# Performance work log

Measured on AMD Instinct MI355X. Metric: run time of the kernel, lower is better.

The kernel has to match this reference:

```python
import jax, jax.numpy as jnp
import numpy as np

NEG = 0.01  # leaky_relu negative slope used throughout AttentiveFP


def _seg_softmax(logits, seg, num):
    # softmax over entries grouped by segment id (PyG softmax w/ 1e-16 eps)
    m = jax.ops.segment_max(logits, seg, num_segments=num)
    m = jnp.where(jnp.isfinite(m), m, 0.0)
    e = jnp.exp(logits - m[seg])
    s = jax.ops.segment_sum(e, seg, num_segments=num)
    return e / (s[seg] + 1e-16)


def _gru(x, h, wi, wh, bi, bh):
    # torch.nn.GRUCell math
    gi = x @ wi.T + bi
    gh = h @ wh.T + bh
    ir, iz, inn = jnp.split(gi, 3, axis=-1)
    hr, hz, hn = jnp.split(gh, 3, axis=-1)
    r = jax.nn.sigmoid(ir + hr)
    z = jax.nn.sigmoid(iz + hz)
    n = jnp.tanh(inn + r * hn)
    return (1.0 - z) * n + z * h


def _forward(x, edge_attr, mol_feats, lin1_w, lin1_b, gate_lin1_w, gate_lin2_w, gate_att_l, gate_att_r, gate_bias, grus_wi, grus_wh, grus_bi, grus_bh, atom_w, atom_att_src, atom_att_dst, atom_bias, mol_w, mol_att_src, mol_att_dst, mol_bias, lin2_w, lin2_b, fcm0_w, fcm0_b, fcm1_w, fcm1_b, fcm2_w, fcm2_b, fc0_w, fc0_b, fc1_w, fc1_b, fc2_w, fc2_b, fc3_w, fc3_b, fc4_w, fc4_b, edge_index, batch):
    N = x.shape[0]
    G = mol_feats.shape[0]
    src, dst = edge_index[0], edge_index[1]
    lrelu = lambda v: jax.nn.leaky_relu(v, NEG)
    # AttentiveFP (eval mode: dropout off)
    xh = lrelu(x @ lin1_w.T + lin1_b)  # [N,H]
    # --- GATEConv: edge-conditioned attention, add aggregation ---
    m = lrelu(jnp.concatenate([xh[src], edge_attr], axis=-1) @ gate_lin1_w.T)  # [E,H]
    a = lrelu(m @ gate_att_l + (xh @ gate_att_r)[dst])
    a = _seg_softmax(a, dst, N)
    h = jax.ops.segment_sum((m @ gate_lin2_w.T) * a[:, None], dst, num_segments=N) + gate_bias
    xh = jax.nn.relu(_gru(jax.nn.elu(h), xh, grus_wi[0], grus_wh[0], grus_bi[0], grus_bh[0]))
    # --- GATConv layers (num_layers-1 = 2, heads=1, no self loops) ---
    for l in range(2):
        xl = xh @ atom_w[l].T
        a = lrelu((xl @ atom_att_src[l])[src] + (xl @ atom_att_dst[l])[dst])
        a = _seg_softmax(a, dst, N)
        h = jax.ops.segment_sum(xl[src] * a[:, None], dst, num_segments=N) + atom_bias[l]
        xh = jax.nn.relu(_gru(jax.nn.elu(h), xh, grus_wi[1 + l], grus_wh[1 + l], grus_bi[1 + l], grus_bh[1 + l]))
    # --- attentive graph readout (num_timesteps = 3) ---
    out = jax.nn.relu(jax.ops.segment_sum(xh, batch, num_segments=G))  # [G,H]
    xm = xh @ mol_w.T            # atom-side lin (x fixed across timesteps)
    a_src = xm @ mol_att_src
    for _ in range(3):
        a = lrelu(a_src + ((out @ mol_w.T) @ mol_att_dst)[batch])
        a = _seg_softmax(a, batch, G)
        h = jax.ops.segment_sum(xm * a[:, None], batch, num_segments=G) + mol_bias
        out = jax.nn.relu(_gru(jax.nn.elu(h), out, grus_wi[3], grus_wh[3], grus_bi[3], grus_bh[3]))
    hg = out @ lin2_w.T + lin2_b  # [G,256]
    # --- mol-feature MLP branch (SiLU) ---
    hm = jax.nn.silu(mol_feats @ fcm0_w.T + fcm0_b)
    hm = jax.nn.silu(hm @ fcm1_w.T + fcm1_b)
    hm = jax.nn.silu(hm @ fcm2_w.T + fcm2_b)
    # --- fusion MLP ---
    hg = jnp.concatenate([hg, hm], axis=1)  # [G,512]
    hg = jax.nn.silu(hg @ fc0_w.T + fc0_b)
    hg = jax.nn.silu(hg @ fc1_w.T + fc1_b)
    hg = jax.nn.silu(hg @ fc2_w.T + fc2_b)
    hg = jax.nn.silu(hg @ fc3_w.T + fc3_b)
    return hg @ fc4_w.T + fc4_b  # [G,1]


def setup_inputs() -> dict:
    key = jax.random.key(0)
    ks = iter(jax.random.split(key, 64))
    def W(*shape):
        return jax.random.normal(next(ks), shape, jnp.float32) / np.float32(np.sqrt(shape[-1]))
    def B(*shape):
        return 0.02 * jax.random.normal(next(ks), shape, jnp.float32)
    N, E, G = 131072, 262144, 8192
    Fn, Fe, Fm, H = 64, 16, 200, 256
    return dict(
        x=jax.random.normal(next(ks), (N, Fn), jnp.float32),
        edge_attr=jax.random.normal(next(ks), (E, Fe), jnp.float32),
        mol_feats=jax.random.normal(next(ks), (G, Fm), jnp.float32),
        lin1_w=W(H, Fn), lin1_b=B(H),
        gate_lin1_w=W(H, H + Fe), gate_lin2_w=W(H, H),
        gate_att_l=W(H), gate_att_r=W(H), gate_bias=B(H),
        grus_wi=W(4, 3 * H, H), grus_wh=W(4, 3 * H, H), grus_bi=B(4, 3 * H), grus_bh=B(4, 3 * H),
        atom_w=W(2, H, H), atom_att_src=W(2, H), atom_att_dst=W(2, H), atom_bias=B(2, H),
        mol_w=W(H, H), mol_att_src=W(H), mol_att_dst=W(H), mol_bias=B(H),
        lin2_w=W(H, H), lin2_b=B(H),
        fcm0_w=W(H, Fm), fcm0_b=B(H), fcm1_w=W(H, H), fcm1_b=B(H), fcm2_w=W(H, H), fcm2_b=B(H),
        fc0_w=W(512, 512), fc0_b=B(512), fc1_w=W(512, 512), fc1_b=B(512),
        fc2_w=W(512, 512), fc2_b=B(512), fc3_w=W(128, 512), fc3_b=B(128),
        fc4_w=W(1, 128), fc4_b=B(1),
        edge_index=jax.random.randint(next(ks), (2, E), 0, N),
        batch=jnp.sort(jax.random.randint(next(ks), (N,), 0, G)),
    )


def reference(x, edge_attr, mol_feats, lin1_w, lin1_b, gate_lin1_w, gate_lin2_w, gate_att_l, gate_att_r, gate_bias, grus_wi, grus_wh, grus_bi, grus_bh, atom_w, atom_att_src, atom_att_dst, atom_bias, mol_w, mol_att_src, mol_att_dst, mol_bias, lin2_w, lin2_b, fcm0_w, fcm0_b, fcm1_w, fcm1_b, fcm2_w, fcm2_b, fc0_w, fc0_b, fc1_w, fc1_b, fc2_w, fc2_b, fc3_w, fc3_b, fc4_w, fc4_b, edge_index, batch):
    return _forward(x, edge_attr, mol_feats, lin1_w, lin1_b, gate_lin1_w, gate_lin2_w, gate_att_l, gate_att_r, gate_bias, grus_wi, grus_wh, grus_bi, grus_bh, atom_w, atom_att_src, atom_att_dst, atom_bias, mol_w, mol_att_src, mol_att_dst, mol_bias, lin2_w, lin2_b, fcm0_w, fcm0_b, fcm1_w, fcm1_b, fcm2_w, fcm2_b, fc0_w, fc0_b, fc1_w, fc1_b, fc2_w, fc2_b, fc3_w, fc3_b, fc4_w, fc4_b, edge_index, batch)
```

## Files before the change

kernel.cpp:

```cpp
#include <hip/hip_runtime.h>
#include <hip/hip_bf16.h>
#include <math.h>


typedef unsigned short u16;
typedef u16 u16x8 __attribute__((ext_vector_type(8)));
typedef short s16x8 __attribute__((ext_vector_type(8)));
typedef float f32x4 __attribute__((ext_vector_type(4)));

__device__ __forceinline__ float u2f(u16 u) { return __uint_as_float(((unsigned)u) << 16); }
__device__ __forceinline__ u16 f2u(float f) {
    return __builtin_bit_cast(u16, __float2bfloat16(f));
}

#define NEGS 0.01f

typedef const __attribute__((address_space(1))) unsigned gas1_t;
typedef __attribute__((address_space(3))) unsigned las3_t;
__device__ __forceinline__ void gload16(const void* g, void* l) {
    __builtin_amdgcn_global_load_lds((gas1_t*)g, (las3_t*)l, 16, 0, 0);
}

__device__ __forceinline__ unsigned fkey(float f) {
    unsigned u = __float_as_uint(f);
    return (u & 0x80000000u) ? ~u : (u | 0x80000000u);
}
__device__ __forceinline__ float funkey(unsigned k) {
    return (k & 0x80000000u) ? __uint_as_float(k ^ 0x80000000u) : __uint_as_float(~k);
}
#define KEY_NEG_INF 0x007FFFFFu

static inline int cdiv(int a, int b) { return (a + b - 1) / b; }

__global__ void fill_f32(float* p, float v, size_t n) {
    size_t i = (size_t)blockIdx.x * 256 + threadIdx.x;
    if (i < n) p[i] = v;
}
__global__ void fill_u32(unsigned* p, unsigned v, int n) {
    int i = blockIdx.x * 256 + threadIdx.x;
    if (i < n) p[i] = v;
}
__global__ void fill_km(unsigned* key, float* sum, int n) {
    int i = blockIdx.x * 256 + threadIdx.x;
    if (i < n) { key[i] = KEY_NEG_INF; sum[i] = 0.f; }
}
__global__ void copy_f2b(const float* s, u16* d, size_t n) {
    size_t i = (size_t)blockIdx.x * 256 + threadIdx.x;
    if (i < n) d[i] = f2u(s[i]);
}
__global__ void matvecT2_k(const float* W1, const float* a1, float* o1,
                           const float* W2, const float* a2, float* o2,
                           int K, int Jout) {
    int j = blockIdx.x * 256 + threadIdx.x;
    if (j < Jout) {
        float s = 0.f;
        for (int k = 0; k < K; k++) s += W1[(size_t)k * Jout + j] * a1[k];
        o1[j] = s;
    } else if (j < 2 * Jout) {
        int jj = j - Jout;
        float s = 0.f;
        for (int k = 0; k < K; k++) s += W2[(size_t)k * Jout + jj] * a2[k];
        o2[jj] = s;
    }
}
__global__ void edge_add_lrelu_max(const float* dp4, float* elog, const float* r,
                                   const int* dsti, unsigned* key, int E) {
    int i = blockIdx.x * 256 + threadIdx.x;
    if (i < E) {
        int d = dsti[i];
        float p = (dp4[i] + dp4[(size_t)E + i]) +
                  (dp4[(size_t)2 * E + i] + dp4[(size_t)3 * E + i]);
        float v = p + r[d];
        v = v > 0.f ? v : NEGS * v;
        elog[i] = v;
        atomicMax(&key[d], fkey(v));
    }
}
__global__ void pair_logit_max(float* elog, const float* s, const float* dd,
                               const int* srci, const int* dsti, unsigned* key, int E) {
    int i = blockIdx.x * 256 + threadIdx.x;
    if (i < E) {
        int d = dsti[i];
        float v = s[srci[i]] + dd[d];
        v = v > 0.f ? v : NEGS * v;
        elog[i] = v;
        atomicMax(&key[d], fkey(v));
    }
}
__global__ void node_logit_max(float* nlog, const float* asrc, const float* wg,
                               const int* batch, unsigned* key, int N) {
    int i = blockIdx.x * 256 + threadIdx.x;
    if (i < N) {
        int b = batch[i];
        float v = asrc[i] + wg[b];
        v = v > 0.f ? v : NEGS * v;
        nlog[i] = v;
        atomicMax(&key[b], fkey(v));
    }
}
__global__ void seg_exp_k(const float* logit, const int* idx, const unsigned* key,
                          float* ex, float* sum, int n) {
    int i = blockIdx.x * 256 + threadIdx.x;
    if (i < n) {
        float e = expf(logit[i] - funkey(key[idx[i]]));
        ex[i] = e;
        atomicAdd(&sum[idx[i]], e);
    }
}
__global__ void rowdot2_b(const u16* X, const float* v1, const float* v2,
                          float* o1, float* o2, int M) {
    int r = blockIdx.x * 4 + (threadIdx.x >> 6);
    int lane = threadIdx.x & 63;
    if (r >= M) return;
    ushort4 rv = *(const ushort4*)(X + (size_t)r * 256 + lane * 4);
    u16 q4[4] = {rv.x, rv.y, rv.z, rv.w};
    float p1 = 0.f, p2 = 0.f;
#pragma unroll
    for (int q = 0; q < 4; q++) {
        float xv = u2f(q4[q]);
        p1 += xv * v1[lane * 4 + q];
        if (v2) p2 += xv * v2[lane * 4 + q];
    }
    for (int off = 32; off; off >>= 1) {
        p1 += __shfl_down(p1, off);
        if (v2) p2 += __shfl_down(p2, off);
    }
    if (lane == 0) {
        o1[r] = p1;
        if (v2) o2[r] = p2;
    }
}
__global__ void rowdot_f(const float* X, const float* v1, float* o1, int M) {
    int r = blockIdx.x * 4 + (threadIdx.x >> 6);
    int lane = threadIdx.x & 63;
    if (r >= M) return;
    float4 a = ((const float4*)(X + (size_t)r * 256))[lane];
    float4 b = ((const float4*)v1)[lane];
    float p1 = a.x * b.x + a.y * b.y + a.z * b.z + a.w * b.w;
    for (int off = 32; off; off >>= 1) p1 += __shfl_down(p1, off);
    if (lane == 0) o1[r] = p1;
}
__global__ void fc4_k(const float* X, const float* w, const float* b, float* out, int G) {
    int g = blockIdx.x * 4 + (threadIdx.x >> 6);
    int lane = threadIdx.x & 63;
    if (g >= G) return;
    float2 xv = ((const float2*)(X + (size_t)g * 128))[lane];
    float2 wv = ((const float2*)w)[lane];
    float p = xv.x * wv.x + xv.y * wv.y;
    for (int off = 32; off; off >>= 1) p += __shfl_down(p, off);
    if (lane == 0) out[g] = p + b[0];
}

__global__ void count_dst(const int* dst, int* cnt, int E) {
    int i = blockIdx.x * 256 + threadIdx.x;
    if (i < E) atomicAdd(&cnt[dst[i]], 1);
}
__global__ void scan1(const int* cnt, int* part, int N) {
    __shared__ int sm[256];
    int i = blockIdx.x * 256 + threadIdx.x;
    sm[threadIdx.x] = i < N ? cnt[i] : 0;
    __syncthreads();
    for (int off = 128; off; off >>= 1) {
        if (threadIdx.x < off) sm[threadIdx.x] += sm[threadIdx.x + off];
        __syncthreads();
    }
    if (threadIdx.x == 0) part[blockIdx.x] = sm[0];
}
__global__ void scan2(int* part, int nb) {
    __shared__ int a[1024], b[1024];
    int t = threadIdx.x;
    if (nb > 1024) {
        if (t == 0) {
            int acc = 0;
            for (int i = 0; i < nb; i++) { int v = part[i]; part[i] = acc; acc += v; }
        }
        return;
    }
    int v = t < nb ? part[t] : 0;
    a[t] = v;
    __syncthreads();
    int* cur = a; int* nxt = b;
    for (int off = 1; off < 1024; off <<= 1) {
        int s = cur[t] + (t >= off ? cur[t - off] : 0);
        nxt[t] = s;
        __syncthreads();
        int* tmp = cur; cur = nxt; nxt = tmp;
    }
    if (t < nb) part[t] = cur[t] - v;
}
__global__ void scan3(const int* cnt, const int* part, int* rowstart, int N) {
    __shared__ int a[256], b[256];
    int t = threadIdx.x;
    int i = blockIdx.x * 256 + t;
    int v = i < N ? cnt[i] : 0;
    a[t] = v;
    __syncthreads();
    int* cur = a; int* nxt = b;
    for (int off = 1; off < 256; off <<= 1) {
        int s = cur[t] + (t >= off ? cur[t - off] : 0);
        nxt[t] = s;
        __syncthreads();
        int* tmp = cur; cur = nxt; nxt = tmp;
    }
    if (i < N) rowstart[i] = part[blockIdx.x] + cur[t] - v;
}
__global__ void fill_csr(const int* dst, const int* rowstart, int* fillc,
                         int* eorder, int E) {
    int e = blockIdx.x * 256 + threadIdx.x;
    if (e >= E) return;
    int d = dst[e];
    int s = rowstart[d] + atomicAdd(&fillc[d], 1);
    eorder[s] = e;
}
__global__ void chunk_dlo_k(const int* rowstart, const int* cnt, int N, int Crows,
                            int nch, int* dlo) {
// ... 299 lines not shown
                    ah[fi], wl[fj], acc[fi][fj], 0, 0, 0);
            }
        __syncthreads();
    }
    const int col = lane & 15, quad = lane >> 4;
    const int n_base = nb * 128 + wn;
    u16* lt = (u16*)lsAll;
    const int rowsM = M - m0;
    if constexpr (EPI == 2) {
        float* dpb = (float*)(lsAll + 2048);
        float dp[4][4] = {};
#pragma unroll
        for (int fi = 0; fi < 4; fi++)
#pragma unroll
            for (int fj = 0; fj < 4; fj++) {
                int nn = n_base + fj * 16 + col;
                float av = attv[nn];
#pragma unroll
                for (int r = 0; r < 4; r++) {
                    float v = actf<ACT>(acc[fi][fj][r]);
                    dp[fi][r] += v * av;
                    if (Cb) {
                        int lr = wm + fi * 16 + quad * 4 + r;
                        int lc = wn + fj * 16 + col;
                        lt[lr * 128 + lc] = f2u(v);
                    }
                }
            }
#pragma unroll
        for (int fi = 0; fi < 4; fi++)
#pragma unroll
            for (int r = 0; r < 4; r++) {
                float p = dp[fi][r];
                p += __shfl_down(p, 8);
                p += __shfl_down(p, 4);
                p += __shfl_down(p, 2);
                p += __shfl_down(p, 1);
                if (col == 0)
                    dpb[((wn >> 6) << 7) + wm + fi * 16 + quad * 4 + r] = p;
            }
        __syncthreads();
        {
            int row = t & 127, sl = t >> 7;
            if (row < rowsM)
                dotout[(size_t)(nb * 2 + sl) * (size_t)M + m0 + row] =
                    dpb[sl * 128 + row];
        }
        if (Cb) {
#pragma unroll
            for (int it = 0; it < 8; it++) {
                int idx = it * 256 + t;
                int row = idx >> 4, c8 = idx & 15;
                if (row < rowsM) {
                    int mm = m0 + row;
                    u16* dst = (mm < csplit) ? Cb + (size_t)mm * 256
                                             : Cb2 + (size_t)(mm - csplit) * 256;
                    ((u16x8*)(dst + nb * 128))[c8] = ((u16x8*)lt)[idx];
                }
            }
        }
    } else if constexpr (EPI == 4) {
#pragma unroll
        for (int fj = 0; fj < 4; fj++) {
            int nn = n_base + fj * 16 + col;
            float bb = b1 ? b1[nn] : 0.f;
#pragma unroll
            for (int fi = 0; fi < 4; fi++)
#pragma unroll
                for (int r = 0; r < 4; r++) {
                    float v = acc[fi][fj][r] + bb;
                    float e = v > 0.f ? v : expm1f(v);
                    int lr = wm + fi * 16 + quad * 4 + r;
                    int lc = wn + fj * 16 + col;
                    lt[lr * 128 + lc] = f2u(e);
                }
        }
        __syncthreads();
#pragma unroll
        for (int it = 0; it < 8; it++) {
            int idx = it * 256 + t;
            int row = idx >> 4, c8 = idx & 15;
            if (row < rowsM)
                ((u16x8*)(Cb + (size_t)(m0 + row) * ldc + nb * 128))[c8] =
                    ((u16x8*)lt)[idx];
        }
        __syncthreads();
#pragma unroll
        for (int fj = 0; fj < 4; fj++) {
            int nn = n_base + fj * 16 + col;
            float bb = b1 ? b1[nn] : 0.f;
#pragma unroll
            for (int fi = 0; fi < 4; fi++)
#pragma unroll
                for (int r = 0; r < 4; r++) {
                    float v = acc[fi][fj][r] + bb;
                    float e = v > 0.f ? v : expm1f(v);
                    u16 hh = f2u(e);
                    int lr = wm + fi * 16 + quad * 4 + r;
                    int lc = wn + fj * 16 + col;
                    lt[lr * 128 + lc] = f2u(e - u2f(hh));
                }
        }
        __syncthreads();
#pragma unroll
        for (int it = 0; it < 8; it++) {
            int idx = it * 256 + t;
            int row = idx >> 4, c8 = idx & 15;
            if (row < rowsM)
                ((u16x8*)(Cb2 + (size_t)(m0 + row) * ldc + nb * 128))[c8] =
                    ((u16x8*)lt)[idx];
        }
    } else if constexpr (EPI == 1) {
#pragma unroll
        for (int fj = 0; fj < 4; fj++) {
            int nn = n_base + fj * 16 + col;
            float bb = b1 ? b1[nn] : 0.f;
#pragma unroll
            for (int fi = 0; fi < 4; fi++)
#pragma unroll
                for (int r = 0; r < 4; r++) {
                    float v = actf<ACT>(acc[fi][fj][r] + bb);
                    int lr = wm + fi * 16 + quad * 4 + r;
                    int lc = wn + fj * 16 + col;
                    lt[lr * 128 + lc] = f2u(v);
                }
        }
        __syncthreads();
#pragma unroll
        for (int it = 0; it < 8; it++) {
            int idx = it * 256 + t;
            int row = idx >> 4, c8 = idx & 15;
            if (row < rowsM)
                ((u16x8*)(Cb + (size_t)(m0 + row) * ldc + nb * 128))[c8] =
                    ((u16x8*)lt)[idx];
        }
    } else {
#pragma unroll
        for (int fj = 0; fj < 4; fj++) {
            int nn = n_base + fj * 16 + col;
            float bb = b1 ? b1[nn] : 0.f;
#pragma unroll
            for (int fi = 0; fi < 4; fi++)
#pragma unroll
                for (int r = 0; r < 4; r++) {
                    int mm = m0 + wm + fi * 16 + quad * 4 + r;
                    if (mm >= M) continue;
                    float v = actf<ACT>(acc[fi][fj][r] + bb);
                    Cf[(size_t)mm * ldc + nn] = v;
                }
        }
    }
}

template <int ALD, bool HB, bool OB>
__global__ __launch_bounds__(256, 4) void mgemm_gru(
    int M, const float* Af, const u16* Ab, const u16* Ab2, const float* X2f,
    const u16* Wp, const float* bp, const u16* hb, const float* hf,
    float* of, u16* ob) {
    __shared__ u16x8 lsAll[2048];
    u16x8* lsAh = lsAll;
    u16x8* lsAl = lsAll + 512;
    u16x8* lsWh = lsAll + 1024;
    u16x8* lsWl = lsAll + 1536;
    const int t = threadIdx.x;
    const int m0 = blockIdx.x * 128;
    const int nb = blockIdx.y;
    const int r0 = ((t >> 6) << 4) | (t & 15);
    const int kq = ((t >> 4) & 3) << 3;
    const int mA[2] = {m0 + r0, m0 + r0 + 64};
    const u16* ehr[2]; const u16* elr[2]; const u16* xhr[2];
    const float* afr[2]; const float* x2r[2];
    bool val[2];
#pragma unroll
    for (int h = 0; h < 2; h++) {
        int m = mA[h];
        val[h] = (m < M);
        int ms = val[h] ? m : 0;
        ehr[h] = nullptr; elr[h] = nullptr; xhr[h] = nullptr;
        afr[h] = nullptr; x2r[h] = nullptr;
        if constexpr (ALD == 5) {
            ehr[h] = Ab + (size_t)ms * 256;
            elr[h] = Ab2 + (size_t)ms * 256;
            xhr[h] = hb + (size_t)ms * 256;
        } else {
            afr[h] = Af + (size_t)ms * 256;
            x2r[h] = X2f + (size_t)ms * 256;
        }
    }
    const int wave = t >> 6, lane = t & 63;
    const int wm = (wave >> 1) << 6, wn = (wave & 1) << 6;
    f32x4 acc[4][4];
#pragma unroll
    for (int i = 0; i < 4; i++)
#pragma unroll
        for (int j = 0; j < 4; j++) {
            acc[i][j][0] = 0.f; acc[i][j][1] = 0.f; acc[i][j][2] = 0.f; acc[i][j][3] = 0.f;
        }
    const u16x8* wh0 = (const u16x8*)Wp + ((size_t)nb * 16 << 9);
    const u16x8* wl0 = (const u16x8*)Wp + (size_t)(8 * 16 * 512) + ((size_t)nb * 16 << 9);
    for (int ki = 0; ki < 16; ki++) {
        int kb = (ki << 5) + kq;
        if constexpr (ALD == 5) {
            const u16* p0 = kb < 256 ? ehr[0] + kb : xhr[0] + (kb - 256);
            const u16* p1 = kb < 256 ? ehr[1] + kb : xhr[1] + (kb - 256);
            gload16(p0, &lsAh[t]);
            gload16(p1, &lsAh[t + 256]);
            if (ki < 8) {
                gload16(elr[0] + kb, &lsAl[t]);
                gload16(elr[1] + kb, &lsAl[t + 256]);
            }
        } else {
            p8 a0 = ldA<4>(val[0], kb, 512, nullptr, afr[0], x2r[0]);
            p8 a1 = ldA<4>(val[1], kb, 512, nullptr, afr[1], x2r[1]);
            lsAh[t] = a0.hi; lsAl[t] = a0.lo;
            lsAh[t + 256] = a1.hi; lsAl[t + 256] = a1.lo;
        }
        const u16x8* wsh = wh0 + ((size_t)ki << 9);
        const u16x8* wsl = wl0 + ((size_t)ki << 9);
        gload16(wsh + t, &lsWh[t]);
        gload16(wsh + t + 256, &lsWh[t + 256]);
        gload16(wsl + t, &lsWl[t]);
        gload16(wsl + t + 256, &lsWl[t + 256]);
        __syncthreads();
        s16x8 ah[4], al[4], wh[4], wl[4];
#pragma unroll
        for (int f = 0; f < 4; f++) {
            int ai = ((wm >> 4) + f) * 64 + lane;
            int wi = ((wn >> 4) + f) * 64 + lane;
            ah[f] = __builtin_bit_cast(s16x8, lsAh[ai]);
            al[f] = __builtin_bit_cast(s16x8, lsAl[ai]);
            wh[f] = __builtin_bit_cast(s16x8, lsWh[wi]);
            wl[f] = __builtin_bit_cast(s16x8, lsWl[wi]);
        }
        bool skip_lh = (ALD == 5) ? (ki >= 8) : false;
        bool hn_zero = (ki < 8);
#pragma unroll
        for (int fi = 0; fi < 4; fi++)
#pragma unroll
            for (int fj = 0; fj < 4; fj++) {
                if (fj == 3 && hn_zero) continue;
                acc[fi][fj] = __builtin_amdgcn_mfma_f32_16x16x32_bf16(
                    ah[fi], wh[fj], acc[fi][fj], 0, 0, 0);
                if (!skip_lh)
                    acc[fi][fj] = __builtin_amdgcn_mfma_f32_16x16x32_bf16(
                        al[fi], wh[fj], acc[fi][fj], 0, 0, 0);
                acc[fi][fj] = __builtin_amdgcn_mfma_f32_16x16x32_bf16(
                    ah[fi], wl[fj], acc[fi][fj], 0, 0, 0);
            }
        __syncthreads();
    }
    const int col = lane & 15, quad = lane >> 4;
    const int nbase = nb * 128 + wn;
    float br = bp[nbase + col];
    float bz = bp[nbase + 16 + col];
    float bn = bp[nbase + 32 + col];
    float bhn = bp[nbase + 48 + col];
    int ch = (nb * 2 + (wn >> 6)) * 16 + col;
    int lc = ((wn >> 6) << 4) + col;
    u16* lt = (u16*)lsAll;
    float* ft = (float*)lsAll;
#pragma unroll
    for (int fi = 0; fi < 4; fi++)
#pragma unroll
        for (int r = 0; r < 4; r++) {
            int m = m0 + wm + fi * 16 + quad * 4 + r;
            if (m >= M) continue;
            float rs = acc[fi][0][r] + br;
            float zs = acc[fi][1][r] + bz;
            float nsv = acc[fi][2][r] + bn;
            float hnv = acc[fi][3][r] + bhn;
            float rr = 1.f / (1.f + expf(-rs));
            float zz = 1.f / (1.f + expf(-zs));
            float nn = tanhf(nsv - hnv + rr * hnv);
            float ho = HB ? u2f(hb[(size_t)m * 256 + ch]) : hf[(size_t)m * 256 + ch];
            float o = fmaxf((1.f - zz) * nn + zz * ho, 0.f);
            int lr = wm + fi * 16 + quad * 4 + r;
            if (OB) lt[lr * 32 + lc] = f2u(o);
            else ft[lr * 32 + lc] = o;
        }
    __syncthreads();
    const int rowsM = M - m0;
    if (OB) {
#pragma unroll
        for (int it = 0; it < 2; it++) {
            int idx = it * 256 + t;
            int row = idx >> 2, c8 = idx & 3;
            if (row < rowsM)
                ((u16x8*)(ob + (size_t)(m0 + row) * 256 + nb * 32))[c8] =
                    ((u16x8*)lt)[idx];
        }
    } else {
#pragma unroll
        for (int it = 0; it < 4; it++) {
            int idx = it * 256 + t;
            int row = idx >> 3, c4 = idx & 7;
            if (row < rowsM)
                ((float4*)(of + (size_t)(m0 + row) * 256 + nb * 32))[c4] =
                    ((float4*)ft)[idx];
        }
    }
}

extern "C" void kernel_launch(void* const* d_in, const int* in_sizes, int n_in,
                              void* d_out, int out_size, void* d_ws, size_t ws_size,
                              hipStream_t stream) {
    const float* x = (const float*)d_in[0];
    const float* edge_attr = (const float*)d_in[1];
    const float* mol_feats = (const float*)d_in[2];
    const float* lin1_w = (const float*)d_in[3];
    const float* lin1_b = (const float*)d_in[4];
    const float* gate_lin1_w = (const float*)d_in[5];
    const float* gate_lin2_w = (const float*)d_in[6];
    const float* gate_att_l = (const float*)d_in[7];
    const float* gate_att_r = (const float*)d_in[8];
    const float* gate_bias = (const float*)d_in[9];
    const float* grus_wi = (const float*)d_in[10];
    const float* grus_wh = (const float*)d_in[11];
    const float* grus_bi = (const float*)d_in[12];
    const float* grus_bh = (const float*)d_in[13];
    const float* atom_w = (const float*)d_in[14];
    const float* atom_att_src = (const float*)d_in[15];
    const float* atom_att_dst = (const float*)d_in[16];
    const float* atom_bias = (const float*)d_in[17];
    const float* mol_w = (const float*)d_in[18];
    const float* mol_att_src = (const float*)d_in[19];
    const float* mol_att_dst = (const float*)d_in[20];
    const float* mol_bias = (const float*)d_in[21];
    const float* lin2_w = (const float*)d_in[22];
    const float* lin2_b = (const float*)d_in[23];
    const float* fcm0_w = (const float*)d_in[24];
    const float* fcm0_b = (const float*)d_in[25];
    const float* fcm1_w = (const float*)d_in[26];
    const float* fcm1_b = (const float*)d_in[27];
    const float* fcm2_w = (const float*)d_in[28];
    const float* fcm2_b = (const float*)d_in[29];
    const float* fc0_w = (const float*)d_in[30];
    const float* fc0_b = (const float*)d_in[31];
    const float* fc1_w = (const float*)d_in[32];
    const float* fc1_b = (const float*)d_in[33];
    const float* fc2_w = (const float*)d_in[34];
    const float* fc2_b = (const float*)d_in[35];
    const float* fc3_w = (const float*)d_in[36];
    const float* fc3_b = (const float*)d_in[37];
    const float* fc4_w = (const float*)d_in[38];
    const float* fc4_b = (const float*)d_in[39];
    const int* edge_index = (const int*)d_in[40];
    const int* batch = (const int*)d_in[41];
    float* out_final = (float*)d_out;

    const int N = in_sizes[0] / 64;
    const int E = in_sizes[1] / 16;
    const int G = in_sizes[2] / 200;
    const int* srcE = edge_index;
    const int* dstE = edge_index + E;

    char* base = (char*)d_ws;
    size_t off = 0;
    auto alloc = [&](size_t bytes) -> char* {
        char* p = base + off;
        off += (bytes + 255) & ~(size_t)255;
        return p;
    };
    u16* xhA = (u16*)alloc((size_t)N * 512);
    u16* haggH = (u16*)alloc((size_t)N * 512);
    u16* haggL = (u16*)alloc((size_t)N * 512);
    float* outg = (float*)alloc((size_t)G * 1024);
    float* hgrb = (float*)alloc((size_t)G * 1024);
    float* elog = (float*)alloc((size_t)E * 4);
    float* eexp = (float*)alloc((size_t)E * 4);
    float* dotp = (float*)alloc((size_t)E * 16);
    unsigned* nkey = (unsigned*)alloc((size_t)N * 4);
    float* nsum = (float*)alloc((size_t)N * 4);
    float* ns1 = (float*)alloc((size_t)N * 4);
    float* ns2 = (float*)alloc((size_t)N * 4);
    unsigned* gkey = (unsigned*)alloc((size_t)G * 4);
    float* gsum = (float*)alloc((size_t)G * 4);
    float* wgb = (float*)alloc((size_t)G * 4);
    float* vbuf = (float*)alloc(4096);
    int* ecnt = (int*)alloc((size_t)N * 4);
    int* efill = (int*)alloc((size_t)N * 4);
    int* erowst = (int*)alloc((size_t)N * 4);
    int* eorder = (int*)alloc((size_t)E * 4);
    int* spart = (int*)alloc(4096 * 4);
    int* cdlo = (int*)alloc(((size_t)E / 128 + 2) * 4);
    int* gs = (int*)alloc((size_t)G * 4);
    int* ge = (int*)alloc((size_t)G * 4);
    u16* pk_lin1 = (u16*)alloc(256 * 64 * 2 * 2);
    u16* pk_g1 = (u16*)alloc(256 * 288 * 2 * 2);
    u16* pk_g2 = (u16*)alloc(256 * 256 * 2 * 2);
    u16* pk_gruF[4];
    float* bp_gru[4];
    for (int l = 0; l < 4; l++) {
        pk_gruF[l] = (u16*)alloc(1024 * 512 * 2 * 2);
        bp_gru[l] = (float*)alloc(1024 * 4);
    }
    u16* pk_atom[2];
    for (int l = 0; l < 2; l++) pk_atom[l] = (u16*)alloc(256 * 256 * 2 * 2);
    u16* pk_mol = (u16*)alloc(256 * 256 * 2 * 2);
    u16* pk_lin2 = (u16*)alloc(256 * 256 * 2 * 2);
    u16* pk_fcm0 = (u16*)alloc(256 * 224 * 2 * 2);
    u16* pk_fcm1 = (u16*)alloc(256 * 256 * 2 * 2);
    u16* pk_fcm2 = (u16*)alloc(256 * 256 * 2 * 2);
    u16* pk_fc0 = (u16*)alloc(512 * 512 * 2 * 2);
    u16* pk_fc1 = (u16*)alloc(512 * 512 * 2 * 2);
    u16* pk_fc2 = (u16*)alloc(512 * 512 * 2 * 2);
    u16* pk_fc3 = (u16*)alloc(128 * 512 * 2 * 2);
    size_t fixed_core = off;
    if (fixed_core + (size_t)2 * 1024 * 1024 > ws_size) {
        fill_f32<<<cdiv(out_size, 256), 256, 0, stream>>>(out_final, (float)ws_size,
                                                          (size_t)out_size);
        return;
    }
    u16* xhB = nullptr;
    bool use_pp = false;
    if (ws_size - off >= (size_t)N * 512 + (size_t)2 * 1024 * 1024) {
        xhB = (u16*)alloc((size_t)N * 512);
        use_pp = true;
    }
    size_t workbytes = ws_size - off;
    char* workp = base + off;
    int Mc = (int)((workbytes / (use_pp ? 1024 : 2048)) & ~(size_t)127);
    if (Mc > N) Mc = N;
    if (Mc < 128) Mc = 128;
    u16* ehi = (u16*)workp;
    u16* elo = ehi + (size_t)Mc * 256;
    float* htmp = (float*)(workp + (size_t)Mc * 1024);
    float* cbuf = (float*)workp;
    u16* mt1 = nullptr; u16* mt2 = nullptr; int msplit = 0x7fffffff;
    if (workbytes >= (size_t)E * 512) { mt1 = (u16*)workp; msplit = E; }
    else if (use_pp) {
        if (N >= E) { mt1 = xhB; msplit = E; }
        else if ((size_t)N * 512 + workbytes >= (size_t)E * 512) {
            mt1 = xhB; msplit = N; mt2 = (u16*)workp;
        }
    }
    bool gate_store = (mt1 != nullptr);
    size_t crows_sz = workbytes / 512;
    if (crows_sz > (size_t)E) crows_sz = (size_t)E;
    int Crows = (int)(crows_sz & ~(size_t)127);
    if (Crows < 128) Crows = 128;
    int nch = cdiv(E, Crows);
    u16* mchunk = (u16*)workp;
    float* fbufA = (float*)haggH;
    float* fbufB = fbufA + (size_t)G * 512;
    float* fbufC = fbufB + (size_t)G * 512;
    float* f128 = fbufC + (size_t)G * 512;
    float* hm1 = f128 + (size_t)G * 128;
    float* hm2 = hm1 + (size_t)G * 256;

    auto pack = [&](const float* s1, const float* s2, int K1, int Ksrc, int Nout,
                    int Kp, u16* dst) {
        int total = (Nout >> 7) * (Kp >> 5) * 512;
        pack_w<<<cdiv(total, 256), 256, 0, stream>>>(s1, s2, K1, Ksrc, Nout, Kp, dst);
    };
    pack(lin1_w, nullptr, 64, 64, 256, 64, pk_lin1);
    pack(gate_lin1_w, nullptr, 272, 272, 256, 288, pk_g1);
    pack(gate_lin2_w, nullptr, 256, 256, 256, 256, pk_g2);
    for (int l = 0; l < 4; l++) {
        pack_gru_w<<<cdiv(8 * 16 * 512, 256), 256, 0, stream>>>(
            grus_wi + (size_t)l * 768 * 256, grus_wh + (size_t)l * 768 * 256,
            pk_gruF[l]);
        pack_gru_b<<<4, 256, 0, stream>>>(grus_bi + (size_t)l * 768,
                                          grus_bh + (size_t)l * 768, bp_gru[l]);
    }
    for (int l = 0; l < 2; l++)
        pack(atom_w + (size_t)l * 256 * 256, nullptr, 256, 256, 256, 256, pk_atom[l]);
    pack(mol_w, nullptr, 256, 256, 256, 256, pk_mol);
    pack(lin2_w, nullptr, 256, 256, 256, 256, pk_lin2);
    pack(fcm0_w, nullptr, 200, 200, 256, 224, pk_fcm0);
    pack(fcm1_w, nullptr, 256, 256, 256, 256, pk_fcm1);
    pack(fcm2_w, nullptr, 256, 256, 256, 256, pk_fcm2);
    pack(fc0_w, nullptr, 512, 512, 512, 512, pk_fc0);
    pack(fc1_w, nullptr, 512, 512, 512, 512, pk_fc1);
    pack(fc2_w, nullptr, 512, 512, 512, 512, pk_fc2);
    pack(fc3_w, nullptr, 512, 512, 128, 512, pk_fc3);

    int nbk = cdiv(N, 256);
    fill_u32<<<nbk, 256, 0, stream>>>((unsigned*)ecnt, 0u, N);
    fill_u32<<<nbk, 256, 0, stream>>>((unsigned*)efill, 0u, N);
    count_dst<<<cdiv(E, 256), 256, 0, stream>>>(dstE, ecnt, E);
    scan1<<<nbk, 256, 0, stream>>>(ecnt, spart, N);
    scan2<<<1, 1024, 0, stream>>>(spart, nbk);
    scan3<<<nbk, 256, 0, stream>>>(ecnt, spart, erowst, N);
    fill_csr<<<cdiv(E, 256), 256, 0, stream>>>(dstE, erowst, efill, eorder, E);
    fill_u32<<<cdiv(G, 256), 256, 0, stream>>>((unsigned*)gs, (unsigned)N, G);
    fill_u32<<<cdiv(G, 256), 256, 0, stream>>>((unsigned*)ge, 0u, G);
    graph_bounds<<<nbk, 256, 0, stream>>>(batch, gs, ge, N);

    u16* xh_cur = xhA;
    u16* xh_nxt = xhB;

    auto node_gru = [&](int l, const u16* Wpre, const float* bpre) {
        for (int c0 = 0; c0 < N; c0 += Mc) {
            int Ms = N - c0 < Mc ? N - c0 : Mc;
            int gx = cdiv(Ms, 128);
            mgemm<6, 0, 4><<<dim3(gx, 2), 256, 0, stream>>>(Ms, 256, 256,
                nullptr, 0, haggH + (size_t)c0 * 256, haggL + (size_t)c0 * 256,
                nullptr, nullptr, Wpre, bpre,
                nullptr, ehi, elo, 0, 256, nullptr, nullptr, nullptr);
            if (use_pp) {
                mgemm_gru<5, true, true><<<dim3(gx, 8), 256, 0, stream>>>(Ms,
                    nullptr, ehi, elo, nullptr, pk_gruF[l], bp_gru[l],
                    xh_cur + (size_t)c0 * 256, nullptr,
                    nullptr, xh_nxt + (size_t)c0 * 256);
            } else {
                mgemm_gru<5, true, false><<<dim3(gx, 8), 256, 0, stream>>>(Ms,
                    nullptr, ehi, elo, nullptr, pk_gruF[l], bp_gru[l],
                    xh_cur + (size_t)c0 * 256, nullptr,
                    htmp, nullptr);
                copy_f2b<<<(int)(((size_t)Ms * 256 + 255) / 256), 256, 0, stream>>>(
                    htmp, xh_cur + (size_t)c0 * 256, (size_t)Ms * 256);
            }
        }
        if (use_pp) { u16* t2 = xh_cur; xh_cur = xh_nxt; xh_nxt = t2; }
    };

    mgemm<1, 1, 1><<<dim3(cdiv(N, 128), 2), 256, 0, stream>>>(N, 64, 64,
        x, 64, nullptr, nullptr, nullptr, nullptr, pk_lin1, lin1_b,
        nullptr, xh_cur, nullptr, 0, 256, nullptr, nullptr, nullptr);

    mgemm<2, 1, 2><<<dim3(cdiv(E, 128), 2), 256, 0, stream>>>(E, 288, 272,
        nullptr, 0, xh_cur, nullptr, srcE, edge_attr, pk_g1, nullptr,
        nullptr, gate_store ? mt1 : nullptr, mt2, msplit, 256,
        gate_att_l, dotp, nullptr);
    rowdot2_b<<<cdiv(N, 4), 256, 0, stream>>>(xh_cur, gate_att_r, nullptr, ns1, nullptr, N);
    fill_km<<<nbk, 256, 0, stream>>>(nkey, nsum, N);
    edge_add_lrelu_max<<<cdiv(E, 256), 256, 0, stream>>>(dotp, elog, ns1, dstE, nkey, E);
    seg_exp_k<<<cdiv(E, 256), 256, 0, stream>>>(elog, dstE, nkey, eexp, nsum, E);
    if (gate_store) {
        csr_red<2><<<N, 256, 0, stream>>>(erowst, ecnt, eorder, eexp, nsum, nullptr,
            mt1, mt2, msplit, 0, E, nullptr, haggH, haggL, N);
    } else {
        fill_u32<<<cdiv(N * 256, 256), 256, 0, stream>>>((unsigned*)haggH, 0u, N * 256);
        chunk_dlo_k<<<cdiv(nch, 64), 64, 0, stream>>>(erowst, ecnt, N, Crows, nch, cdlo);
        for (int c = 0; c < nch; c++) {
            int s0 = c * Crows;
            int s1 = s0 + Crows < E ? s0 + Crows : E;
            int Ms = s1 - s0;
            mgemm<7, 1, 1><<<dim3(cdiv(Ms, 128), 2), 256, 0, stream>>>(Ms, 288, 272,
                nullptr, 0, xh_cur, nullptr, eorder + s0, edge_attr, pk_g1, nullptr,
                nullptr, mchunk, nullptr, 0x7fffffff, 256,
                nullptr, nullptr, srcE);
            csr_red<1><<<Crows, 256, 0, stream>>>(erowst, ecnt, eorder, eexp, nsum,
                nullptr, mchunk, nullptr, 0, s0, s1, cdlo + c, haggH, haggL, N);
        }
    }
    node_gru(0, pk_g2, gate_bias);

    for (int l = 0; l < 2; l++) {
        const float* aw = atom_w + (size_t)l * 256 * 256;
        matvecT2_k<<<2, 256, 0, stream>>>(aw, atom_att_src + (size_t)l * 256, vbuf,
                                          aw, atom_att_dst + (size_t)l * 256, vbuf + 256,
                                          256, 256);
        rowdot2_b<<<cdiv(N, 4), 256, 0, stream>>>(xh_cur, vbuf, vbuf + 256, ns1, ns2, N);
        fill_km<<<nbk, 256, 0, stream>>>(nkey, nsum, N);
        pair_logit_max<<<cdiv(E, 256), 256, 0, stream>>>(elog, ns1, ns2, srcE, dstE, nkey, E);
        seg_exp_k<<<cdiv(E, 256), 256, 0, stream>>>(elog, dstE, nkey, eexp, nsum, E);
        csr_red<0><<<N, 256, 0, stream>>>(erowst, ecnt, eorder, eexp, nsum, srcE,
            xh_cur, nullptr, 0, 0, 0, nullptr, haggH, haggL, N);
        node_gru(1 + l, pk_atom[l], atom_bias + (size_t)l * 256);
    }

    seg_red<true><<<G, 256, 0, stream>>>(gs, ge, xh_cur, nullptr, nullptr, outg, G);
    matvecT2_k<<<2, 256, 0, stream>>>(mol_w, mol_att_dst, vbuf,
                                      mol_w, mol_att_src, vbuf + 256, 256, 256);
    rowdot2_b<<<cdiv(N, 4), 256, 0, stream>>>(xh_cur, vbuf + 256, nullptr, ns1, nullptr, N);
    float* ogc = outg;
    float* ogn = hgrb;
    int McG = Mc < G ? Mc : G;
    for (int t = 0; t < 3; t++) {
        rowdot_f<<<cdiv(G, 4), 256, 0, stream>>>(ogc, vbuf, wgb, G);
        fill_km<<<cdiv(G, 256), 256, 0, stream>>>(gkey, gsum, G);
        node_logit_max<<<nbk, 256, 0, stream>>>(elog, ns1, wgb, batch, gkey, N);
        seg_exp_k<<<nbk, 256, 0, stream>>>(elog, batch, gkey, eexp, gsum, N);
        seg_red<false><<<G, 256, 0, stream>>>(gs, ge, xh_cur, eexp, gsum, ogn, G);
        for (int c0 = 0; c0 < G; c0 += McG) {
            int Ms = G - c0 < McG ? G - c0 : McG;
            int gx = cdiv(Ms, 128);
            mgemm<1, 0, 0><<<dim3(gx, 2), 256, 0, stream>>>(Ms, 256, 256,
                ogn + (size_t)c0 * 256, 256, nullptr, nullptr, nullptr, nullptr,
                pk_mol, mol_bias, cbuf, nullptr, nullptr, 0, 256,
                nullptr, nullptr, nullptr);
            mgemm_gru<4, false, false><<<dim3(gx, 8), 256, 0, stream>>>(Ms,
                cbuf, nullptr, nullptr, ogc + (size_t)c0 * 256, pk_gruF[3], bp_gru[3],
                nullptr, ogc + (size_t)c0 * 256, ogn + (size_t)c0 * 256, nullptr);
        }
        float* tt = ogc; ogc = ogn; ogn = tt;
    }

    int gG = cdiv(G, 128);
    mgemm<1, 0, 0><<<dim3(gG, 2), 256, 0, stream>>>(G, 256, 256, ogc, 256,
        nullptr, nullptr, nullptr, nullptr, pk_lin2, lin2_b,
        fbufA, nullptr, nullptr, 0, 512, nullptr, nullptr, nullptr);
    mgemm<1, 3, 0><<<dim3(gG, 2), 256, 0, stream>>>(G, 224, 200, mol_feats, 200,
        nullptr, nullptr, nullptr, nullptr, pk_fcm0, fcm0_b,
        hm1, nullptr, nullptr, 0, 256, nullptr, nullptr, nullptr);
    mgemm<1, 3, 0><<<dim3(gG, 2), 256, 0, stream>>>(G, 256, 256, hm1, 256,
        nullptr, nullptr, nullptr, nullptr, pk_fcm1, fcm1_b,
        hm2, nullptr, nullptr, 0, 256, nullptr, nullptr, nullptr);
    mgemm<1, 3, 0><<<dim3(gG, 2), 256, 0, stream>>>(G, 256, 256, hm2, 256,
        nullptr, nullptr, nullptr, nullptr, pk_fcm2, fcm2_b,
        fbufA + 256, nullptr, nullptr, 0, 512, nullptr, nullptr, nullptr);
    mgemm<1, 3, 0><<<dim3(gG, 4), 256, 0, stream>>>(G, 512, 512, fbufA, 512,
        nullptr, nullptr, nullptr, nullptr, pk_fc0, fc0_b,
        fbufB, nullptr, nullptr, 0, 512, nullptr, nullptr, nullptr);
    mgemm<1, 3, 0><<<dim3(gG, 4), 256, 0, stream>>>(G, 512, 512, fbufB, 512,
        nullptr, nullptr, nullptr, nullptr, pk_fc1, fc1_b,
        fbufC, nullptr, nullptr, 0, 512, nullptr, nullptr, nullptr);
    mgemm<1, 3, 0><<<dim3(gG, 4), 256, 0, stream>>>(G, 512, 512, fbufC, 512,
        nullptr, nullptr, nullptr, nullptr, pk_fc2, fc2_b,
        fbufB, nullptr, nullptr, 0, 512, nullptr, nullptr, nullptr);
    mgemm<1, 3, 0><<<dim3(gG, 1), 256, 0, stream>>>(G, 512, 512, fbufB, 512,
        nullptr, nullptr, nullptr, nullptr, pk_fc3, fc3_b,
        f128, nullptr, nullptr, 0, 128, nullptr, nullptr, nullptr);
    fc4_k<<<cdiv(G, 4), 256, 0, stream>>>(f128, fc4_w, fc4_b, out_final, G);
}
```

Measured before the change: 5.444 ms.

## Fuse attention row-dot products into GRU epilogue with partial-sum planes

The attention projections (xh·v_src, xh·v_dst) that were computed by separate rowdot passes over the node features are now computed inside the mgemm_gru epilogue. Each block writes its 32-column partial dot into one of 16 planes, and a small plane_sum16 kernel reduces them. The matvec weight-attention vectors are precomputed once up front. This removes a full re-read of the N×256 node features per layer, at the cost of extra shuffles, LDS, partial-sum traffic and an extra launch.

```diff
diff --git a/kernel.cpp b/kernel.cpp
--- a/kernel.cpp
+++ b/kernel.cpp
@@ -61,6 +61,20 @@
         float s = 0.f;
         for (int k = 0; k < K; k++) s += W2[(size_t)k * Jout + jj] * a2[k];
         o2[jj] = s;
+    }
+}
+__global__ void plane_sum16(const float* p1, const float* p2, float* o1, float* o2,
+                            int ldpl, int n) {
+    int i = blockIdx.x * 256 + threadIdx.x;
+    if (i < n) {
+        float s = 0.f;
+        for (int k = 0; k < 16; k++) s += p1[(size_t)k * ldpl + i];
+        o1[i] = s;
+        if (p2) {
+            float s2 = 0.f;
+            for (int k = 0; k < 16; k++) s2 += p2[(size_t)k * ldpl + i];
+            o2[i] = s2;
+        }
     }
 }
 __global__ void edge_add_lrelu_max(const float* dp4, float* elog, const float* r,
@@ -666,12 +680,13 @@
     }
 }
 
-template <int ALD, bool HB, bool OB>
+template <int ALD, bool HB, bool OB, bool DOTS>
 __global__ __launch_bounds__(256, 4) void mgemm_gru(
     int M, const float* Af, const u16* Ab, const u16* Ab2, const float* X2f,
     const u16* Wp, const float* bp, const u16* hb, const float* hf,
-    float* of, u16* ob) {
-    __shared__ u16x8 lsAll[2048];
+    float* of, u16* ob,
+    const float* dv1, const float* dv2, float* dpl1, float* dpl2, int ldpl) {
+    __shared__ u16x8 lsAll[2176];
     u16x8* lsAh = lsAll;
     u16x8* lsAl = lsAll + 512;
     u16x8* lsWh = lsAll + 1024;
@@ -773,11 +788,19 @@
     int lc = ((wn >> 6) << 4) + col;
     u16* lt = (u16*)lsAll;
     float* ft = (float*)lsAll;
+    float* dpq = (float*)(lsAll + 2048);
+    float vA = 0.f, vB = 0.f;
+    if (DOTS) {
+        vA = dv1[ch];
+        if (dv2) vB = dv2[ch];
+    }
+    float d1[4][4], d2[4][4];
 #pragma unroll
     for (int fi = 0; fi < 4; fi++)
 #pragma unroll
         for (int r = 0; r < 4; r++) {
             int m = m0 + wm + fi * 16 + quad * 4 + r;
+            if (DOTS) { d1[fi][r] = 0.f; d2[fi][r] = 0.f; }
             if (m >= M) continue;
             float rs = acc[fi][0][r] + br;
             float zs = acc[fi][1][r] + bz;
@@ -791,9 +814,44 @@
             int lr = wm + fi * 16 + quad * 4 + r;
             if (OB) lt[lr * 32 + lc] = f2u(o);
             else ft[lr * 32 + lc] = o;
-        }
+            if (DOTS) {
+                float ob16 = u2f(f2u(o));
+                d1[fi][r] = ob16 * vA;
+                d2[fi][r] = ob16 * vB;
+            }
+        }
+    if (DOTS) {
+#pragma unroll
+        for (int fi = 0; fi < 4; fi++)
+#pragma unroll
+            for (int r = 0; r < 4; r++) {
+                float p = d1[fi][r];
+                p += __shfl_down(p, 8);
+                p += __shfl_down(p, 4);
+                p += __shfl_down(p, 2);
+                p += __shfl_down(p, 1);
+                float q = d2[fi][r];
+                q += __shfl_down(q, 8);
+                q += __shfl_down(q, 4);
+                q += __shfl_down(q, 2);
+                q += __shfl_down(q, 1);
+                if (col == 0) {
+                    int lr = wm + fi * 16 + quad * 4 + r;
+                    dpq[((wn >> 6) << 7) + lr] = p;
+                    dpq[256 + ((wn >> 6) << 7) + lr] = q;
+                }
+            }
+    }
     __syncthreads();
     const int rowsM = M - m0;
+    if (DOTS) {
+        int half = t >> 7, row = t & 127;
+        if (row < rowsM) {
+            size_t pi = (size_t)(nb * 2 + half) * (size_t)ldpl + m0 + row;
+            dpl1[pi] = dpq[(half << 7) + row];
+            if (dpl2) dpl2[pi] = dpq[256 + (half << 7) + row];
+        }
+    }
     if (OB) {
 #pragma unroll
         for (int it = 0; it < 2; it++) {
@@ -890,7 +948,7 @@
     unsigned* gkey = (unsigned*)alloc((size_t)G * 4);
     float* gsum = (float*)alloc((size_t)G * 4);
     float* wgb = (float*)alloc((size_t)G * 4);
-    float* vbuf = (float*)alloc(4096);
+    float* vbuf = (float*)alloc(8192);
     int* ecnt = (int*)alloc((size_t)N * 4);
     int* efill = (int*)alloc((size_t)N * 4);
     int* erowst = (int*)alloc((size_t)N * 4);
@@ -955,6 +1013,9 @@
     if (Crows < 128) Crows = 128;
     int nch = cdiv(E, Crows);
     u16* mchunk = (u16*)workp;
+    float* dpl1 = outg;
+    float* dpl2 = hgrb;
+    bool fuse_dots = use_pp && ((size_t)16 * N * 4 <= (size_t)G * 1024);
     float* fbufA = (float*)haggH;
     float* fbufB = fbufA + (size_t)G * 512;
     float* fbufC = fbufB + (size_t)G * 512;
@@ -989,6 +1050,14 @@
     pack(fc2_w, nullptr, 512, 512, 512, 512, pk_fc2);
     pack(fc3_w, nullptr, 512, 512, 128, 512, pk_fc3);
 
+    matvecT2_k<<<2, 256, 0, stream>>>(atom_w, atom_att_src, vbuf,
+                                      atom_w, atom_att_dst, vbuf + 256, 256, 256);
+    matvecT2_k<<<2, 256, 0, stream>>>(atom_w + 65536, atom_att_src + 256, vbuf + 512,
+                                      atom_w + 65536, atom_att_dst + 256, vbuf + 768,
+                                      256, 256);
+    matvecT2_k<<<2, 256, 0, stream>>>(mol_w, mol_att_dst, vbuf + 1024,
+                                      mol_w, mol_att_src, vbuf + 1280, 256, 256);
+
     int nbk = cdiv(N, 256);
     fill_u32<<<nbk, 256, 0, stream>>>((unsigned*)ecnt, 0u, N);
     fill_u32<<<nbk, 256, 0, stream>>>((unsigned*)efill, 0u, N);
@@ -1004,7 +1073,8 @@
     u16* xh_cur = xhA;
     u16* xh_nxt = xhB;
 
-    auto node_gru = [&](int l, const u16* Wpre, const float* bpre) {
+    auto node_gru = [&](int l, const u16* Wpre, const float* bpre,
+                        const float* dv1, const float* dv2) {
         for (int c0 = 0; c0 < N; c0 += Mc) {
             int Ms = N - c0 < Mc ? N - c0 : Mc;
             int gx = cdiv(Ms, 128);
@@ -1013,15 +1083,24 @@
                 nullptr, nullptr, Wpre, bpre,
                 nullptr, ehi, elo, 0, 256, nullptr, nullptr, nullptr);
             if (use_pp) {
-                mgemm_gru<5, true, true><<<dim3(gx, 8), 256, 0, stream>>>(Ms,
+                if (fuse_dots && dv1) {
+                    mgemm_gru<5, true, true, true><<<dim3(gx, 8), 256, 0, stream>>>(Ms,
+                        nullptr, ehi, elo, nullptr, pk_gruF[l], bp_gru[l],
+                        xh_cur + (size_t)c0 * 256, nullptr,
+                        nullptr, xh_nxt + (size_t)c0 * 256,
+                        dv1, dv2, dpl1 + c0, dv2 ? dpl2 + c0 : nullptr, N);
+                } else {
+                    mgemm_gru<5, true, true, false><<<dim3(gx, 8), 256, 0, stream>>>(Ms,
+                        nullptr, ehi, elo, nullptr, pk_gruF[l], bp_gru[l],
+                        xh_cur + (size_t)c0 * 256, nullptr,
+                        nullptr, xh_nxt + (size_t)c0 * 256,
+                        nullptr, nullptr, nullptr, nullptr, 0);
+                }
+            } else {
+                mgemm_gru<5, true, false, false><<<dim3(gx, 8), 256, 0, stream>>>(Ms,
                     nullptr, ehi, elo, nullptr, pk_gruF[l], bp_gru[l],
                     xh_cur + (size_t)c0 * 256, nullptr,
-                    nullptr, xh_nxt + (size_t)c0 * 256);
-            } else {
-                mgemm_gru<5, true, false><<<dim3(gx, 8), 256, 0, stream>>>(Ms,
-                    nullptr, ehi, elo, nullptr, pk_gruF[l], bp_gru[l],
-                    xh_cur + (size_t)c0 * 256, nullptr,
-                    htmp, nullptr);
+                    htmp, nullptr, nullptr, nullptr, nullptr, nullptr, 0);
                 copy_f2b<<<(int)(((size_t)Ms * 256 + 255) / 256), 256, 0, stream>>>(
                     htmp, xh_cur + (size_t)c0 * 256, (size_t)Ms * 256);
             }
@@ -1059,31 +1138,40 @@
                 nullptr, mchunk, nullptr, 0, s0, s1, cdlo + c, haggH, haggL, N);
         }
     }
-    node_gru(0, pk_g2, gate_bias);
+    node_gru(0, pk_g2, gate_bias, fuse_dots ? vbuf : nullptr, vbuf + 256);
+    if (fuse_dots)
+        plane_sum16<<<nbk, 256, 0, stream>>>(dpl1, dpl2, ns1, ns2, N, N);
 
     for (int l = 0; l < 2; l++) {
-        const float* aw = atom_w + (size_t)l * 256 * 256;
-        matvecT2_k<<<2, 256, 0, stream>>>(aw, atom_att_src + (size_t)l * 256, vbuf,
-                                          aw, atom_att_dst + (size_t)l * 256, vbuf + 256,
-                                          256, 256);
-        rowdot2_b<<<cdiv(N, 4), 256, 0, stream>>>(xh_cur, vbuf, vbuf + 256, ns1, ns2, N);
+        if (!fuse_dots) {
+            const float* vs = vbuf + l * 512;
+            rowdot2_b<<<cdiv(N, 4), 256, 0, stream>>>(xh_cur, vs, vs + 256, ns1, ns2, N);
+        }
         fill_km<<<nbk, 256, 0, stream>>>(nkey, nsum, N);
         pair_logit_max<<<cdiv(E, 256), 256, 0, stream>>>(elog, ns1, ns2, srcE, dstE, nkey, E);
         seg_exp_k<<<cdiv(E, 256), 256, 0, stream>>>(elog, dstE, nkey, eexp, nsum, E);
         csr_red<0><<<N, 256, 0, stream>>>(erowst, ecnt, eorder, eexp, nsum, srcE,
             xh_cur, nullptr, 0, 0, 0, nullptr, haggH, haggL, N);
-        node_gru(1 + l, pk_atom[l], atom_bias + (size_t)l * 256);
-    }
-
+        const float* ndv1 = nullptr; const float* ndv2 = nullptr;
+        if (fuse_dots) {
+            if (l == 0) { ndv1 = vbuf + 512; ndv2 = vbuf + 768; }
+            else { ndv1 = vbuf + 1280; ndv2 = nullptr; }
+        }
+        node_gru(1 + l, pk_atom[l], atom_bias + (size_t)l * 256, ndv1, ndv2);
+        if (fuse_dots)
+            plane_sum16<<<nbk, 256, 0, stream>>>(dpl1, (l == 0) ? dpl2 : nullptr,
+                                                 ns1, (l == 0) ? ns2 : nullptr, N, N);
+    }
+
+    if (!fuse_dots)
+        rowdot2_b<<<cdiv(N, 4), 256, 0, stream>>>(xh_cur, vbuf + 1280, nullptr,
+                                                  ns1, nullptr, N);
     seg_red<true><<<G, 256, 0, stream>>>(gs, ge, xh_cur, nullptr, nullptr, outg, G);
-    matvecT2_k<<<2, 256, 0, stream>>>(mol_w, mol_att_dst, vbuf,
-                                      mol_w, mol_att_src, vbuf + 256, 256, 256);
-    rowdot2_b<<<cdiv(N, 4), 256, 0, stream>>>(xh_cur, vbuf + 256, nullptr, ns1, nullptr, N);
     float* ogc = outg;
     float* ogn = hgrb;
     int McG = Mc < G ? Mc : G;
     for (int t = 0; t < 3; t++) {
-        rowdot_f<<<cdiv(G, 4), 256, 0, stream>>>(ogc, vbuf, wgb, G);
+        rowdot_f<<<cdiv(G, 4), 256, 0, stream>>>(ogc, vbuf + 1024, wgb, G);
         fill_km<<<cdiv(G, 256), 256, 0, stream>>>(gkey, gsum, G);
         node_logit_max<<<nbk, 256, 0, stream>>>(elog, ns1, wgb, batch, gkey, N);
         seg_exp_k<<<nbk, 256, 0, stream>>>(elog, batch, gkey, eexp, gsum, N);
@@ -1095,9 +1183,10 @@
                 ogn + (size_t)c0 * 256, 256, nullptr, nullptr, nullptr, nullptr,
                 pk_mol, mol_bias, cbuf, nullptr, nullptr, 0, 256,
                 nullptr, nullptr, nullptr);
-            mgemm_gru<4, false, false><<<dim3(gx, 8), 256, 0, stream>>>(Ms,
+            mgemm_gru<4, false, false, false><<<dim3(gx, 8), 256, 0, stream>>>(Ms,
                 cbuf, nullptr, nullptr, ogc + (size_t)c0 * 256, pk_gruF[3], bp_gru[3],
-                nullptr, ogc + (size_t)c0 * 256, ogn + (size_t)c0 * 256, nullptr);
+                nullptr, ogc + (size_t)c0 * 256, ogn + (size_t)c0 * 256, nullptr,
+                nullptr, nullptr, nullptr, nullptr, 0);
         }
         float* tt = ogc; ogc = ogn; ogn = tt;
     }
```

Result: slower. 5.584 ms (+2.6%).
